# Kernel tuning notes

Measured on AMD Instinct MI355X. Metric: run time of the kernel, lower is better.

The kernel has to match this reference:

```python
import jax, jax.numpy as jnp
import numpy as np

B, F0, D = 4096, 39, 16
CIN = [128, 128, 128]


def setup_inputs() -> dict:
    key = jax.random.key(0)
    ks = jax.random.split(key, 4)
    x = jax.random.normal(ks[0], (B, F0, D), dtype=jnp.float32)
    fields = [F0] + CIN
    inp = {"embedded_features": x}
    for i in range(len(CIN)):
        cin = F0 * fields[i]
        cout = fields[i + 1]
        kw = jax.random.fold_in(ks[1], i)
        # Conv1d default init scale ~ 1/sqrt(fan_in)
        inp[f"W{i}"] = jax.random.normal(kw, (cout, cin), dtype=jnp.float32) / np.sqrt(cin)
        inp[f"b{i}"] = jnp.zeros((cout,), dtype=jnp.float32)
    return inp


def _cin_layer(X0, Xi, W, b):
    # Math identical to: outer_product [B,F0,Fi,D] -> reshape [B,F0*Fi,D] -> 1x1 Conv1d.
    # Conv1d(kernel=1) over the flattened F0*Fi channel dim is a contraction over (j,k):
    #   Xn[b,h,d] = sum_{j,k} W[h, j*Fi+k] * X0[b,j,d] * Xi[b,k,d] + b[h]
    H = W.shape[0]
    F0_, Fi = X0.shape[1], Xi.shape[1]
    Wr = W.reshape(H, F0_, Fi)
    return jnp.einsum('hjk,bjd,bkd->bhd', Wr, X0, Xi) + b[None, :, None]


def reference(embedded_features, W0, b0, W1, b1, W2, b2):
    X0 = embedded_features  # [B, F0, D]
    Ws = [(W0, b0), (W1, b1), (W2, b2)]
    Xi = X0
    res = []
    for W, b in Ws:
        Xi = _cin_layer(X0, Xi, W, b)  # [B, H_i, D]
        res.append(Xi.sum(axis=2))     # sum over embedding dim
    return jnp.concatenate(res, axis=1)  # [B, sum(cin_size)]
```

## Files before the change

### kernel.cpp

```cpp
#include <hip/hip_runtime.h>
#include <stdint.h>


#define NB_F0 39
#define NB_H  128
#define NB_B  4096
#define XROW 130

typedef float f32x4  __attribute__((ext_vector_type(4)));
typedef float f32x16 __attribute__((ext_vector_type(16)));
typedef short s16x8  __attribute__((ext_vector_type(8)));

template <int N> struct IC { static constexpr int value = N; };

__device__ __forceinline__ unsigned short rne_bf16(float f) {
  union { float f; unsigned u; } v; v.f = f;
  return (unsigned short)((v.u + 0x7fffu + ((v.u >> 16) & 1u)) >> 16);
}

__global__ void prep_all_kernel(const float* __restrict__ X0g,
                                unsigned short* __restrict__ X0T,
                                float* __restrict__ X0f,
                                const float* __restrict__ W0s,
                                unsigned short* __restrict__ Wf0,
                                const float* __restrict__ W1s,
                                unsigned short* __restrict__ Wf1,
                                const float* __restrict__ W2s,
                                unsigned short* __restrict__ Wf2) {
  const int t = threadIdx.x;
  int blk = blockIdx.x;
  if (blk < NB_B) {
    const int b = blk;
    {
      const int d  = t >> 4;
      const int k4 = (t & 15) << 2;
      unsigned short vv[4];
#pragma unroll
      for (int i = 0; i < 4; ++i) {
        const int k = k4 + i;
        vv[i] = (k < NB_F0)
                    ? rne_bf16(X0g[(size_t)b * (NB_F0 * 16) + k * 16 + d])
                    : (unsigned short)0;
      }
      ushort4 pk; pk.x = vv[0]; pk.y = vv[1]; pk.z = vv[2]; pk.w = vv[3];
      *(ushort4*)&X0T[((size_t)b * 16 + d) * 64 + k4] = pk;
    }
    for (int idx = t; idx < NB_F0 * 16; idx += 256) {
      const int j = idx >> 4, pos = idx & 15;
      const int d =
          (pos & 3) | (((pos >> 3) & 1) << 2) | (((pos >> 2) & 1) << 3);
      X0f[(size_t)b * (NB_F0 * 16) + idx] =
          X0g[(size_t)b * (NB_F0 * 16) + j * 16 + d];
    }
    return;
  }
  blk -= NB_B;
  constexpr int TW0  = NB_F0 * 4 * 4 * 512;
  constexpr int TW12 = NB_F0 * 4 * 8 * 512;
  constexpr int NB0  = TW0 / 256;
  constexpr int NB12 = TW12 / 256;
  const float* Wsrc; unsigned short* Wdst; int Fi, kshift, idx;
  if (blk < NB0) {
    Wsrc = W0s; Wdst = Wf0; Fi = 39;  kshift = 2; idx = blk * 256 + t;
  } else if (blk < NB0 + NB12) {
    Wsrc = W1s; Wdst = Wf1; Fi = 128; kshift = 3;
    idx = (blk - NB0) * 256 + t;
  } else {
    Wsrc = W2s; Wdst = Wf2; Fi = 128; kshift = 3;
    idx = (blk - NB0 - NB12) * 256 + t;
  }
  const int i    = idx & 7;
  const int lane = (idx >> 3) & 63;
  const int c    = (idx >> 9) & ((1 << kshift) - 1);
  const int jt   = idx >> (9 + kshift);
  const int tt   = jt & 3;
  const int j    = jt >> 2;
  const int h = tt * 32 + (lane & 31);
  const int k = c * 16 + ((lane >> 5) << 3) + i;
  unsigned short v = 0;
  if (k < Fi) v = rne_bf16(Wsrc[(size_t)h * (NB_F0 * Fi) + j * Fi + k]);
  Wdst[idx] = v;
}

__global__ __launch_bounds__(256, 1) void cin_fused(
    const unsigned short* __restrict__ Wf0,
    const unsigned short* __restrict__ Wf1,
    const unsigned short* __restrict__ Wf2,
    const unsigned short* __restrict__ X0T,
    const float* __restrict__ X0f,
    const float* __restrict__ bias0,
    const float* __restrict__ bias1,
    const float* __restrict__ bias2,
    float* __restrict__ outp)
{
  __shared__ __attribute__((aligned(16))) float x0f[4 * NB_F0 * 16];
  __shared__ __attribute__((aligned(16))) unsigned short Xa[4 * 16 * XROW];
  __shared__ __attribute__((aligned(16))) unsigned short Xb[4 * 16 * XROW];

  const int tid  = threadIdx.x;
  const int lane = tid & 63;
  const int wv   = tid >> 6;
  const int L    = lane >> 5;
  const int col  = lane & 31;
  const int bblk = blockIdx.x * 4;

  {
    const float* src = X0f + (size_t)bblk * (NB_F0 * 16);
    for (int c = tid; c < (4 * NB_F0 * 16) / 4; c += 256)
      *(f32x4*)&x0f[c * 4] = *(const f32x4*)&src[c * 4];
  }
  __syncthreads();

  const int x0base = L * 8;

  auto layer = [&](auto kc, auto ast, const unsigned short* __restrict__ Wl,
                   const unsigned short* af_base, const float* __restrict__ bv,
                   float* __restrict__ op, unsigned short* xn) {
    constexpr int KC16 = decltype(kc)::value;
    constexpr int AST  = decltype(ast)::value;

    s16x8 af[2][KC16];
#pragma unroll
    for (int P = 0; P < 2; ++P) {
      const unsigned short* base = af_base +
          (size_t)(2 * P + (col >> 4)) * (16 * AST) + (col & 15) * AST + L * 8;
#pragma unroll
      for (int c = 0; c < KC16; ++c) af[P][c] = *(const s16x8*)(base + c * 16);
    }

    f32x16 Xacc[2], kZero;
#pragma unroll
    for (int r = 0; r < 16; ++r) kZero[r] = 0.f;
#pragma unroll
    for (int P = 0; P < 2; ++P) Xacc[P] = kZero;

    const s16x8* __restrict__ W8 = (const s16x8*)Wl;
    auto wload = [&](int j, s16x8 (&w)[KC16]) {
      const s16x8* p = W8 + ((size_t)(j * 4 + wv) * KC16) * 64 + lane;
#pragma unroll
      for (int c = 0; c < KC16; ++c) w[c] = p[c * 64];
    };

    auto compute = [&](int s, const s16x8 (&w)[KC16]) {
#pragma unroll
      for (int P = 0; P < 2; ++P) {
        f32x16 y = __builtin_amdgcn_mfma_f32_32x32x16_bf16(af[P][0], w[0],
                                                           kZero, 0, 0, 0);
#pragma unroll
        for (int c = 1; c < KC16; ++c)
          y = __builtin_amdgcn_mfma_f32_32x32x16_bf16(af[P][c], w[c], y,
                                                      0, 0, 0);
        const float* xr0 = &x0f[x0base + (2 * P + 0) * (NB_F0 * 16) + s * 16];
        const float* xr1 = &x0f[x0base + (2 * P + 1) * (NB_F0 * 16) + s * 16];
        const f32x4 a0 = *(const f32x4*)(xr0);
        const f32x4 a1 = *(const f32x4*)(xr0 + 4);
        const f32x4 a2 = *(const f32x4*)(xr1);
        const f32x4 a3 = *(const f32x4*)(xr1 + 4);
        f32x16 xsc;
#pragma unroll
        for (int i = 0; i < 4; ++i) {
          xsc[i]      = a0[i];
          xsc[4 + i]  = a1[i];
          xsc[8 + i]  = a2[i];
          xsc[12 + i] = a3[i];
        }
        Xacc[P] = __builtin_elementwise_fma(xsc, y, Xacc[P]);
      }
    };

    s16x8 wA[KC16], wB[KC16];
    wload(0, wA);
    wload(1, wB);
    int s = 0;
    for (; s + 2 <= NB_F0; s += 2) {
      compute(s, wA);
      wload(s + 2 < NB_F0 ? s + 2 : 0, wA);
      compute(s + 1, wB);
      if (s + 3 < NB_F0) wload(s + 3, wB);
    }
    if (s < NB_F0) compute(s, wA);

    const float bias_v = bv[wv * 32 + col];
#pragma unroll
    for (int P = 0; P < 2; ++P) {
#pragma unroll
      for (int bh = 0; bh < 2; ++bh) {
        const int bl = 2 * P + bh;
        float v[8];
#pragma unroll
        for (int m = 0; m < 8; ++m) v[m] = Xacc[P][bh * 8 + m] + bias_v;
        if (xn) {
#pragma unroll
          for (int m = 0; m < 8; ++m) {
            const int d = (m & 3) + 8 * ((m >> 2) & 1) + 4 * L;
            xn[(bl * 16 + d) * XROW + wv * 32 + col] = rne_bf16(v[m]);
          }
        }
        float tot = ((v[0] + v[1]) + (v[2] + v[3])) +
                    ((v[4] + v[5]) + (v[6] + v[7]));
        tot += __shfl_xor(tot, 32);
        if (lane < 32) op[(size_t)(bblk + bl) * 384 + wv * 32 + lane] = tot;
      }
    }
  };

  layer(IC<4>{}, IC<64>{}, Wf0, X0T + (size_t)bblk * (16 * 64),
        bias0, outp + 0, Xa);
  __syncthreads();
  layer(IC<8>{}, IC<XROW>{}, Wf1, Xa, bias1, outp + 128, Xb);
  __syncthreads();
  layer(IC<8>{}, IC<XROW>{}, Wf2, Xb, bias2, outp + 256,
        (unsigned short*)nullptr);
}

extern "C" void kernel_launch(void* const* d_in, const int* in_sizes, int n_in,
                              void* d_out, int out_size, void* d_ws, size_t ws_size,
                              hipStream_t stream) {
  (void)in_sizes; (void)n_in; (void)out_size; (void)ws_size;
  const float* X0g = (const float*)d_in[0];
  const float* W0  = (const float*)d_in[1];
  const float* b0  = (const float*)d_in[2];
  const float* W1  = (const float*)d_in[3];
  const float* b1  = (const float*)d_in[4];
  const float* W2  = (const float*)d_in[5];
  const float* b2  = (const float*)d_in[6];
  float* out = (float*)d_out;

  char* p = (char*)d_ws;
  unsigned short* X0T = (unsigned short*)p; p += (size_t)NB_B * 16 * 64 * 2;
  float*          X0f = (float*)p;          p += (size_t)NB_B * NB_F0 * 16 * 4;
  unsigned short* Wf0 = (unsigned short*)p; p += (size_t)NB_F0 * 4 * 4 * 512 * 2;
  unsigned short* Wf1 = (unsigned short*)p; p += (size_t)NB_F0 * 4 * 8 * 512 * 2;
  unsigned short* Wf2 = (unsigned short*)p; p += (size_t)NB_F0 * 4 * 8 * 512 * 2;

  constexpr int TW0  = NB_F0 * 4 * 4 * 512;
  constexpr int TW12 = NB_F0 * 4 * 8 * 512;
  const int prep_blocks = NB_B + TW0 / 256 + 2 * (TW12 / 256);
  hipLaunchKernelGGL(prep_all_kernel, dim3(prep_blocks), dim3(256), 0, stream,
                     X0g, X0T, X0f, W0, Wf0, W1, Wf1, W2, Wf2);

  hipLaunchKernelGGL(cin_fused, dim3(NB_B / 4), dim3(256), 0, stream,
                     Wf0, Wf1, Wf2, X0T, X0f, b0, b1, b2, out);
}
```

Before: 296.5 us.

## Split batch pairs across two wave groups with 512-thread blocks

The fused CIN kernel now runs 8 waves per block instead of 4. Each wave handles one 32-row H tile and one pair of batch rows, where before each wave looped over both pairs. This halves per-wave accumulator and A-fragment registers and doubles the waves available to hide MFMA and load latency. In exchange, each weight fragment is loaded from global or L2 by two waves instead of one, which doubles weight read traffic per block.

```diff
diff --git a/kernel.cpp b/kernel.cpp
--- a/kernel.cpp
+++ b/kernel.cpp
@@ -82,7 +82,7 @@
   Wdst[idx] = v;
 }
 
-__global__ __launch_bounds__(256, 1) void cin_fused(
+__global__ __launch_bounds__(512, 1) void cin_fused(
     const unsigned short* __restrict__ Wf0,
     const unsigned short* __restrict__ Wf1,
     const unsigned short* __restrict__ Wf2,
@@ -100,13 +100,15 @@
   const int tid  = threadIdx.x;
   const int lane = tid & 63;
   const int wv   = tid >> 6;
+  const int ht   = wv & 3;
+  const int bp   = wv >> 2;
   const int L    = lane >> 5;
   const int col  = lane & 31;
   const int bblk = blockIdx.x * 4;
 
   {
     const float* src = X0f + (size_t)bblk * (NB_F0 * 16);
-    for (int c = tid; c < (4 * NB_F0 * 16) / 4; c += 256)
+    for (int c = tid; c < (4 * NB_F0 * 16) / 4; c += 512)
       *(f32x4*)&x0f[c * 4] = *(const f32x4*)&src[c * 4];
   }
   __syncthreads();
@@ -119,53 +121,47 @@
     constexpr int KC16 = decltype(kc)::value;
     constexpr int AST  = decltype(ast)::value;
 
-    s16x8 af[2][KC16];
-#pragma unroll
-    for (int P = 0; P < 2; ++P) {
+    s16x8 af[KC16];
+    {
       const unsigned short* base = af_base +
-          (size_t)(2 * P + (col >> 4)) * (16 * AST) + (col & 15) * AST + L * 8;
-#pragma unroll
-      for (int c = 0; c < KC16; ++c) af[P][c] = *(const s16x8*)(base + c * 16);
-    }
-
-    f32x16 Xacc[2], kZero;
+          (size_t)(2 * bp + (col >> 4)) * (16 * AST) + (col & 15) * AST + L * 8;
+#pragma unroll
+      for (int c = 0; c < KC16; ++c) af[c] = *(const s16x8*)(base + c * 16);
+    }
+
+    f32x16 Xacc, kZero;
 #pragma unroll
     for (int r = 0; r < 16; ++r) kZero[r] = 0.f;
-#pragma unroll
-    for (int P = 0; P < 2; ++P) Xacc[P] = kZero;
+    Xacc = kZero;
 
     const s16x8* __restrict__ W8 = (const s16x8*)Wl;
     auto wload = [&](int j, s16x8 (&w)[KC16]) {
-      const s16x8* p = W8 + ((size_t)(j * 4 + wv) * KC16) * 64 + lane;
+      const s16x8* p = W8 + ((size_t)(j * 4 + ht) * KC16) * 64 + lane;
 #pragma unroll
       for (int c = 0; c < KC16; ++c) w[c] = p[c * 64];
     };
 
     auto compute = [&](int s, const s16x8 (&w)[KC16]) {
-#pragma unroll
-      for (int P = 0; P < 2; ++P) {
-        f32x16 y = __builtin_amdgcn_mfma_f32_32x32x16_bf16(af[P][0], w[0],
-                                                           kZero, 0, 0, 0);
-#pragma unroll
-        for (int c = 1; c < KC16; ++c)
-          y = __builtin_amdgcn_mfma_f32_32x32x16_bf16(af[P][c], w[c], y,
-                                                      0, 0, 0);
-        const float* xr0 = &x0f[x0base + (2 * P + 0) * (NB_F0 * 16) + s * 16];
-        const float* xr1 = &x0f[x0base + (2 * P + 1) * (NB_F0 * 16) + s * 16];
-        const f32x4 a0 = *(const f32x4*)(xr0);
-        const f32x4 a1 = *(const f32x4*)(xr0 + 4);
-        const f32x4 a2 = *(const f32x4*)(xr1);
-        const f32x4 a3 = *(const f32x4*)(xr1 + 4);
-        f32x16 xsc;
-#pragma unroll
-        for (int i = 0; i < 4; ++i) {
-          xsc[i]      = a0[i];
-          xsc[4 + i]  = a1[i];
-          xsc[8 + i]  = a2[i];
-          xsc[12 + i] = a3[i];
-        }
-        Xacc[P] = __builtin_elementwise_fma(xsc, y, Xacc[P]);
+      f32x16 y = __builtin_amdgcn_mfma_f32_32x32x16_bf16(af[0], w[0],
+                                                         kZero, 0, 0, 0);
+#pragma unroll
+      for (int c = 1; c < KC16; ++c)
+        y = __builtin_amdgcn_mfma_f32_32x32x16_bf16(af[c], w[c], y, 0, 0, 0);
+      const float* xr0 = &x0f[x0base + (2 * bp + 0) * (NB_F0 * 16) + s * 16];
+      const float* xr1 = &x0f[x0base + (2 * bp + 1) * (NB_F0 * 16) + s * 16];
+      const f32x4 a0 = *(const f32x4*)(xr0);
+      const f32x4 a1 = *(const f32x4*)(xr0 + 4);
+      const f32x4 a2 = *(const f32x4*)(xr1);
+      const f32x4 a3 = *(const f32x4*)(xr1 + 4);
+      f32x16 xsc;
+#pragma unroll
+      for (int i = 0; i < 4; ++i) {
+        xsc[i]      = a0[i];
+        xsc[4 + i]  = a1[i];
+        xsc[8 + i]  = a2[i];
+        xsc[12 + i] = a3[i];
       }
+      Xacc = __builtin_elementwise_fma(xsc, y, Xacc);
     };
 
     s16x8 wA[KC16], wB[KC16];
@@ -180,27 +176,24 @@
     }
     if (s < NB_F0) compute(s, wA);
 
-    const float bias_v = bv[wv * 32 + col];
-#pragma unroll
-    for (int P = 0; P < 2; ++P) {
-#pragma unroll
-      for (int bh = 0; bh < 2; ++bh) {
-        const int bl = 2 * P + bh;
-        float v[8];
-#pragma unroll
-        for (int m = 0; m < 8; ++m) v[m] = Xacc[P][bh * 8 + m] + bias_v;
-        if (xn) {
-#pragma unroll
-          for (int m = 0; m < 8; ++m) {
-            const int d = (m & 3) + 8 * ((m >> 2) & 1) + 4 * L;
-            xn[(bl * 16 + d) * XROW + wv * 32 + col] = rne_bf16(v[m]);
-          }
+    const float bias_v = bv[ht * 32 + col];
+#pragma unroll
+    for (int bh = 0; bh < 2; ++bh) {
+      const int bl = 2 * bp + bh;
+      float v[8];
+#pragma unroll
+      for (int m = 0; m < 8; ++m) v[m] = Xacc[bh * 8 + m] + bias_v;
+      if (xn) {
+#pragma unroll
+        for (int m = 0; m < 8; ++m) {
+          const int d = (m & 3) + 8 * ((m >> 2) & 1) + 4 * L;
+          xn[(bl * 16 + d) * XROW + ht * 32 + col] = rne_bf16(v[m]);
         }
-        float tot = ((v[0] + v[1]) + (v[2] + v[3])) +
-                    ((v[4] + v[5]) + (v[6] + v[7]));
-        tot += __shfl_xor(tot, 32);
-        if (lane < 32) op[(size_t)(bblk + bl) * 384 + wv * 32 + lane] = tot;
       }
+      float tot = ((v[0] + v[1]) + (v[2] + v[3])) +
+                  ((v[4] + v[5]) + (v[6] + v[7]));
+      tot += __shfl_xor(tot, 32);
+      if (lane < 32) op[(size_t)(bblk + bl) * 384 + ht * 32 + lane] = tot;
     }
   };
 
@@ -239,6 +232,6 @@
   hipLaunchKernelGGL(prep_all_kernel, dim3(prep_blocks), dim3(256), 0, stream,
                      X0g, X0T, X0f, W0, Wf0, W1, Wf1, W2, Wf2);
 
-  hipLaunchKernelGGL(cin_fused, dim3(NB_B / 4), dim3(256), 0, stream,
+  hipLaunchKernelGGL(cin_fused, dim3(NB_B / 4), dim3(512), 0, stream,
                      Wf0, Wf1, Wf2, X0T, X0f, b0, b1, b2, out);
 }
```

New measurement: 328.2 us. +10.7%, slower.

## Split K across two wave groups with LDS reduction in fused CIN kernel

Applied to the files above, without the earlier changes.

Doubles the block to 512 threads (8 waves). Each group of four waves computes the same 128 output rows over half of the contraction chunks, then adds the two halves' partial accumulators through LDS scratch that reuses the existing Xa/Xb buffers. The goal is more waves in flight to hide the latency of weight loads and MFMA chains, and fewer A-fragment and weight registers per wave. The cost is extra barriers, LDS traffic for the partial sums, and the x0 scaling FMA now done in both halves.

```diff
diff --git a/kernel.cpp b/kernel.cpp
--- a/kernel.cpp
+++ b/kernel.cpp
@@ -82,7 +82,7 @@
   Wdst[idx] = v;
 }
 
-__global__ __launch_bounds__(256, 1) void cin_fused(
+__global__ __launch_bounds__(512, 1) void cin_fused(
     const unsigned short* __restrict__ Wf0,
     const unsigned short* __restrict__ Wf1,
     const unsigned short* __restrict__ Wf2,
@@ -100,13 +100,15 @@
   const int tid  = threadIdx.x;
   const int lane = tid & 63;
   const int wv   = tid >> 6;
+  const int ht   = wv & 3;
+  const int kh   = wv >> 2;
   const int L    = lane >> 5;
   const int col  = lane & 31;
   const int bblk = blockIdx.x * 4;
 
   {
     const float* src = X0f + (size_t)bblk * (NB_F0 * 16);
-    for (int c = tid; c < (4 * NB_F0 * 16) / 4; c += 256)
+    for (int c = tid; c < (4 * NB_F0 * 16) / 4; c += 512)
       *(f32x4*)&x0f[c * 4] = *(const f32x4*)&src[c * 4];
   }
   __syncthreads();
@@ -115,18 +117,22 @@
 
   auto layer = [&](auto kc, auto ast, const unsigned short* __restrict__ Wl,
                    const unsigned short* af_base, const float* __restrict__ bv,
-                   float* __restrict__ op, unsigned short* xn) {
+                   float* __restrict__ op, unsigned short* xn,
+                   float* redsc, bool afbar) {
     constexpr int KC16 = decltype(kc)::value;
+    constexpr int KCh  = KC16 / 2;
     constexpr int AST  = decltype(ast)::value;
 
-    s16x8 af[2][KC16];
+    s16x8 af[2][KCh];
 #pragma unroll
     for (int P = 0; P < 2; ++P) {
       const unsigned short* base = af_base +
-          (size_t)(2 * P + (col >> 4)) * (16 * AST) + (col & 15) * AST + L * 8;
-#pragma unroll
-      for (int c = 0; c < KC16; ++c) af[P][c] = *(const s16x8*)(base + c * 16);
-    }
+          (size_t)(2 * P + (col >> 4)) * (16 * AST) + (col & 15) * AST +
+          kh * (KCh * 16) + L * 8;
+#pragma unroll
+      for (int c = 0; c < KCh; ++c) af[P][c] = *(const s16x8*)(base + c * 16);
+    }
+    if (afbar) __syncthreads();
 
     f32x16 Xacc[2], kZero;
 #pragma unroll
@@ -135,19 +141,20 @@
     for (int P = 0; P < 2; ++P) Xacc[P] = kZero;
 
     const s16x8* __restrict__ W8 = (const s16x8*)Wl;
-    auto wload = [&](int j, s16x8 (&w)[KC16]) {
-      const s16x8* p = W8 + ((size_t)(j * 4 + wv) * KC16) * 64 + lane;
-#pragma unroll
-      for (int c = 0; c < KC16; ++c) w[c] = p[c * 64];
+    auto wload = [&](int j, s16x8 (&w)[KCh]) {
+      const s16x8* p =
+          W8 + ((size_t)(j * 4 + ht) * KC16 + kh * KCh) * 64 + lane;
+#pragma unroll
+      for (int c = 0; c < KCh; ++c) w[c] = p[c * 64];
     };
 
-    auto compute = [&](int s, const s16x8 (&w)[KC16]) {
+    auto compute = [&](int s, const s16x8 (&w)[KCh]) {
 #pragma unroll
       for (int P = 0; P < 2; ++P) {
         f32x16 y = __builtin_amdgcn_mfma_f32_32x32x16_bf16(af[P][0], w[0],
                                                            kZero, 0, 0, 0);
 #pragma unroll
-        for (int c = 1; c < KC16; ++c)
+        for (int c = 1; c < KCh; ++c)
           y = __builtin_amdgcn_mfma_f32_32x32x16_bf16(af[P][c], w[c], y,
                                                       0, 0, 0);
         const float* xr0 = &x0f[x0base + (2 * P + 0) * (NB_F0 * 16) + s * 16];
@@ -168,7 +175,7 @@
       }
     };
 
-    s16x8 wA[KC16], wB[KC16];
+    s16x8 wA[KCh], wB[KCh];
     wload(0, wA);
     wload(1, wB);
     int s = 0;
@@ -180,37 +187,57 @@
     }
     if (s < NB_F0) compute(s, wA);
 
-    const float bias_v = bv[wv * 32 + col];
 #pragma unroll
     for (int P = 0; P < 2; ++P) {
-#pragma unroll
-      for (int bh = 0; bh < 2; ++bh) {
-        const int bl = 2 * P + bh;
-        float v[8];
-#pragma unroll
-        for (int m = 0; m < 8; ++m) v[m] = Xacc[P][bh * 8 + m] + bias_v;
-        if (xn) {
-#pragma unroll
-          for (int m = 0; m < 8; ++m) {
-            const int d = (m & 3) + 8 * ((m >> 2) & 1) + 4 * L;
-            xn[(bl * 16 + d) * XROW + wv * 32 + col] = rne_bf16(v[m]);
+      if (kh == 1) {
+#pragma unroll
+        for (int r = 0; r < 16; ++r)
+          redsc[(ht * 16 + r) * 64 + lane] = Xacc[P][r];
+      }
+      __syncthreads();
+      if (kh == 0) {
+#pragma unroll
+        for (int r = 0; r < 16; ++r)
+          Xacc[P][r] += redsc[(ht * 16 + r) * 64 + lane];
+      }
+      __syncthreads();
+    }
+
+    if (kh == 0) {
+      const float bias_v = bv[ht * 32 + col];
+#pragma unroll
+      for (int P = 0; P < 2; ++P) {
+#pragma unroll
+        for (int bh = 0; bh < 2; ++bh) {
+          const int bl = 2 * P + bh;
+          float v[8];
+#pragma unroll
+          for (int m = 0; m < 8; ++m) v[m] = Xacc[P][bh * 8 + m] + bias_v;
+          if (xn) {
+#pragma unroll
+            for (int m = 0; m < 8; ++m) {
+              const int d = (m & 3) + 8 * ((m >> 2) & 1) + 4 * L;
+              xn[(bl * 16 + d) * XROW + ht * 32 + col] = rne_bf16(v[m]);
+            }
           }
+          float tot = ((v[0] + v[1]) + (v[2] + v[3])) +
+                      ((v[4] + v[5]) + (v[6] + v[7]));
+          tot += __shfl_xor(tot, 32);
+          if (lane < 32)
+            op[(size_t)(bblk + bl) * 384 + ht * 32 + lane] = tot;
         }
-        float tot = ((v[0] + v[1]) + (v[2] + v[3])) +
-                    ((v[4] + v[5]) + (v[6] + v[7]));
-        tot += __shfl_xor(tot, 32);
-        if (lane < 32) op[(size_t)(bblk + bl) * 384 + wv * 32 + lane] = tot;
       }
     }
   };
 
   layer(IC<4>{}, IC<64>{}, Wf0, X0T + (size_t)bblk * (16 * 64),
-        bias0, outp + 0, Xa);
+        bias0, outp + 0, Xa, (float*)Xb, false);
   __syncthreads();
-  layer(IC<8>{}, IC<XROW>{}, Wf1, Xa, bias1, outp + 128, Xb);
+  layer(IC<8>{}, IC<XROW>{}, Wf1, Xa, bias1, outp + 128, Xb,
+        (float*)Xa, true);
   __syncthreads();
   layer(IC<8>{}, IC<XROW>{}, Wf2, Xb, bias2, outp + 256,
-        (unsigned short*)nullptr);
+        (unsigned short*)nullptr, (float*)Xa, false);
 }
 
 extern "C" void kernel_launch(void* const* d_in, const int* in_sizes, int n_in,
@@ -239,6 +266,6 @@
   hipLaunchKernelGGL(prep_all_kernel, dim3(prep_blocks), dim3(256), 0, stream,
                      X0g, X0T, X0f, W0, Wf0, W1, Wf1, W2, Wf2);
 
-  hipLaunchKernelGGL(cin_fused, dim3(NB_B / 4), dim3(256), 0, stream,
+  hipLaunchKernelGGL(cin_fused, dim3(NB_B / 4), dim3(512), 0, stream,
                      Wf0, Wf1, Wf2, X0T, X0f, b0, b1, b2, out);
 }
```

After: 309.7 us. 4.4% more time.
